# Kernel optimization log

Measured on AMD Instinct MI355X. Metric: run time of the kernel, lower is better.

The kernel has to match this reference:

```python
import jax, jax.numpy as jnp
import numpy as np

# Standard NF4 lookup table (16 quantile values of a normal distribution)
NF4_TABLE = jnp.array([
    -1.0, -0.6961928009986877, -0.5250730514526367, -0.39491748809814453,
    -0.28444138169288635, -0.18477343022823334, -0.09105003625154495, 0.0,
    0.07958029955625534, 0.16093020141124725, 0.24611230194568634,
    0.33791524171829224, 0.44070982933044434, 0.5626170039176941,
    0.7229568362236023, 1.0], dtype=jnp.float32)
BLOCK = 64  # per-block quantization block size


def dequant_nf4(codes, scalers):
    """codes: int [out, in] values in [0,16); scalers: float [out*in/BLOCK]."""
    shape = codes.shape
    vals = NF4_TABLE[codes.reshape(-1, BLOCK)]  # [n_blocks, BLOCK]
    return (vals * scalers[:, None]).reshape(shape)


def setup_inputs() -> dict:
    key = jax.random.key(0)
    ks = jax.random.split(key, 7)
    D, H, T = 4096, 11008, 8192
    nb1 = H * D // BLOCK
    x = jax.random.normal(ks[0], (T, D), dtype=jnp.float32)
    w1_codes = jax.random.randint(ks[1], (H, D), 0, 16, dtype=jnp.int32)
    w1_scalers = jax.random.uniform(ks[2], (nb1,), dtype=jnp.float32) * 0.02
    w2_codes = jax.random.randint(ks[3], (H, D), 0, 16, dtype=jnp.int32)
    w2_scalers = jax.random.uniform(ks[4], (nb1,), dtype=jnp.float32) * 0.02
    w3_codes = jax.random.randint(ks[5], (D, H), 0, 16, dtype=jnp.int32)
    w3_scalers = jax.random.uniform(ks[6], (nb1,), dtype=jnp.float32) * 0.02
    return {"x": x, "w1_codes": w1_codes, "w1_scalers": w1_scalers,
            "w2_codes": w2_codes, "w2_scalers": w2_scalers,
            "w3_codes": w3_codes, "w3_scalers": w3_scalers}


def reference(x, w1_codes, w1_scalers, w2_codes, w2_scalers, w3_codes, w3_scalers):
    w1 = dequant_nf4(w1_codes, w1_scalers)  # [H, D]
    w2 = dequant_nf4(w2_codes, w2_scalers)  # [H, D]
    w3 = dequant_nf4(w3_codes, w3_scalers)  # [D, H]
    h = jax.nn.silu(x @ w1.T) * (x @ w2.T)  # [T, H]
    return h @ w3.T                          # [T, D]
```

## Files before the change

### kernel.cpp

```cpp
#include <hip/hip_runtime.h>
#include <hip/hip_bf16.h>

#define T_DIM 8192
#define D_DIM 4096
#define H_DIM 11008

typedef __attribute__((ext_vector_type(8))) __bf16 bf16x8;
typedef __attribute__((ext_vector_type(4))) float f32x4;

typedef __attribute__((address_space(1))) const void gvoid_t;
typedef __attribute__((address_space(3))) void lvoid_t;

__device__ __forceinline__ void async_lds16(const void* g, void* l) {
    __builtin_amdgcn_global_load_lds((gvoid_t*)g, (lvoid_t*)l, 16, 0, 0);
}

__device__ const float NF4_TAB[16] = {
    -1.0f, -0.6961928009986877f, -0.5250730514526367f, -0.39491748809814453f,
    -0.28444138169288635f, -0.18477343022823334f, -0.09105003625154495f, 0.0f,
    0.07958029955625534f, 0.16093020141124725f, 0.24611230194568634f,
    0.33791524171829224f, 0.44070982933044434f, 0.5626170039176941f,
    0.7229568362236023f, 1.0f};

__global__ void dequant_nf4_kernel(const int* __restrict__ codes,
                                   const float* __restrict__ scalers,
                                   __bf16* __restrict__ out, long n) {
    __shared__ float tbl[16];
    if (threadIdx.x < 16) tbl[threadIdx.x] = NF4_TAB[threadIdx.x];
    __syncthreads();
    long i = ((long)blockIdx.x * blockDim.x + threadIdx.x) * 8;
    if (i >= n) return;
    float s = scalers[i >> 6];
    const int4* cp = (const int4*)(codes + i);
    int4 c0 = cp[0], c1 = cp[1];
    bf16x8 v;
    v[0] = (__bf16)(tbl[c0.x] * s);
    v[1] = (__bf16)(tbl[c0.y] * s);
    v[2] = (__bf16)(tbl[c0.z] * s);
    v[3] = (__bf16)(tbl[c0.w] * s);
    v[4] = (__bf16)(tbl[c1.x] * s);
    v[5] = (__bf16)(tbl[c1.y] * s);
    v[6] = (__bf16)(tbl[c1.z] * s);
    v[7] = (__bf16)(tbl[c1.w] * s);
    *(bf16x8*)(out + i) = v;
}

__global__ void cvt_f32_bf16(const float* __restrict__ x, __bf16* __restrict__ out, long n) {
    long i = ((long)blockIdx.x * blockDim.x + threadIdx.x) * 8;
    if (i >= n) return;
    const float4* xp = (const float4*)(x + i);
    float4 f0 = xp[0], f1 = xp[1];
    bf16x8 v;
    v[0] = (__bf16)f0.x; v[1] = (__bf16)f0.y; v[2] = (__bf16)f0.z; v[3] = (__bf16)f0.w;
    v[4] = (__bf16)f1.x; v[5] = (__bf16)f1.y; v[6] = (__bf16)f1.z; v[7] = (__bf16)f1.w;
    *(bf16x8*)(out + i) = v;
}

template<int KD, int FUSE, typename OutT>
__global__ __launch_bounds__(512, 2) void gemm_nt(
    const __bf16* __restrict__ A, const __bf16* __restrict__ B,
    const __bf16* __restrict__ A1, OutT* __restrict__ Out, const int N)
{
    static_assert(KD % 128 == 0, "need an even number of K-tiles");
    __shared__ __bf16 lds[2 * 2 * 256 * 64];

    const int tid  = threadIdx.x;
    const int lane = tid & 63;
    const int wave = tid >> 6;
    const int wm = wave >> 2;
    const int wn = wave & 3;

    const int nwg  = gridDim.x * gridDim.y;
    const int bid0 = blockIdx.y * gridDim.x + blockIdx.x;
    const int bid  = (bid0 & 7) * (nwg >> 3) + (bid0 >> 3);
    const int bx = bid % gridDim.x;
    const int by = bid / gridDim.x;
    const long m0 = (long)by * 256;
    const long n0 = (long)bx * 256;

    const int sr = tid >> 3;
    const int sb = (tid & 7) ^ (sr & 7);
    const __bf16* Arow = A + (m0 + sr) * (long)KD + sb * 8;
    const __bf16* Brow = B + (n0 + sr) * (long)KD + sb * 8;
    __bf16* dstA = &lds[(wave << 3) * 64];
    __bf16* dstB = dstA + 16384;

#define STAGE_A(BUF, H, KT) do { \
        const __bf16* s_ = Arow + (long)(H) * 128 * KD + (long)(KT) * 64; \
        __bf16* d_ = dstA + (BUF) * 32768 + (H) * 8192; \
        async_lds16(s_, d_); \
        async_lds16(s_ + 64 * (long)KD, d_ + 4096); \
    } while (0)
#define STAGE_B(BUF, H, KT) do { \
        const __bf16* s_ = Brow + (long)(H) * 128 * KD + (long)(KT) * 64; \
        __bf16* d_ = dstB + (BUF) * 32768 + (H) * 8192; \
        async_lds16(s_, d_); \
        async_lds16(s_ + 64 * (long)KD, d_ + 4096); \
    } while (0)

    const int r15 = lane & 15;
    const int hi2 = lane >> 4;
    const int l7  = lane & 7;
    const int aOff = (wm * 128 + r15) * 64;
    const int bOff = 16384 + (wn * 64 + r15) * 64;

    auto rdA = [&](int buf, int m, int kk) -> bf16x8 {
        return *(const bf16x8*)&lds[buf * 32768 + aOff + m * 1024 +
                                    (((kk * 4 + hi2) ^ l7) << 3)];
    };
    auto rdB = [&](int buf, int n, int kk) -> bf16x8 {
        return *(const bf16x8*)&lds[buf * 32768 + bOff + n * 1024 +
                                    (((kk * 4 + hi2) ^ l7) << 3)];
    };

    f32x4 acc[8][4];
    const f32x4 z4 = {0.f, 0.f, 0.f, 0.f};
#pragma unroll
    for (int m = 0; m < 8; ++m)
#pragma unroll
        for (int n = 0; n < 4; ++n) acc[m][n] = z4;

    bf16x8 aF[4][2];
    bf16x8 bF[4][2];

#define LOAD_A4(BUF, MB) { _Pragma("unroll") for (int m_ = 0; m_ < 4; ++m_) { \
        aF[m_][0] = rdA(BUF, m_ + MB, 0); aF[m_][1] = rdA(BUF, m_ + MB, 1); } }
#define LOAD_B2(BUF, NB) { _Pragma("unroll") for (int n_ = 0; n_ < 2; ++n_) { \
        bF[n_ + NB][0] = rdB(BUF, n_ + NB, 0); bF[n_ + NB][1] = rdB(BUF, n_ + NB, 1); } }
#define QUAD(MB, NB) { _Pragma("unroll") for (int m_ = 0; m_ < 4; ++m_) { \
        _Pragma("unroll") for (int n_ = 0; n_ < 2; ++n_) { \
        acc[m_ + MB][n_ + NB] = __builtin_amdgcn_mfma_f32_16x16x32_bf16( \
            aF[m_][0], bF[n_ + NB][0], acc[m_ + MB][n_ + NB], 0, 0, 0); \
        acc[m_ + MB][n_ + NB] = __builtin_amdgcn_mfma_f32_16x16x32_bf16( \
            aF[m_][1], bF[n_ + NB][1], acc[m_ + MB][n_ + NB], 0, 0, 0); } } }
#define BAR()  __builtin_amdgcn_s_barrier()
#define LGK0() asm volatile("s_waitcnt lgkmcnt(0)" ::: "memory")
#define VM4()  asm volatile("s_waitcnt vmcnt(4)" ::: "memory")
#define PRIO1() __builtin_amdgcn_s_setprio(1)
#define PRIO0() __builtin_amdgcn_s_setprio(0)

    const int NT = KD / 64;

    STAGE_A(0, 0, 0); STAGE_A(0, 1, 0);
    STAGE_B(0, 0, 0); STAGE_B(0, 1, 0);
    STAGE_B(1, 0, 1); STAGE_B(1, 1, 1);
    VM4();
    BAR();

#pragma unroll 1
    for (int t = 0; t < NT; t += 2) {
        const int t1 = t + 1;
        int t2 = t + 2; if (t2 >= NT) t2 -= NT;
        int t3 = t + 3; if (t3 >= NT) t3 -= NT;

        LOAD_A4(0, 0); LOAD_B2(0, 0);
        STAGE_A(1, 0, t1);
        BAR(); LGK0();
        PRIO1(); QUAD(0, 0); PRIO0();
        BAR();

        LOAD_B2(0, 2);
        STAGE_A(1, 1, t1);
        BAR(); LGK0();
        PRIO1(); QUAD(0, 2); PRIO0();
        BAR();

        LOAD_A4(0, 4);
        STAGE_B(0, 0, t2);
        BAR(); LGK0();
        PRIO1(); QUAD(4, 2); PRIO0();
        BAR();

        STAGE_B(0, 1, t2);
        BAR();
        PRIO1(); QUAD(4, 0); PRIO0();
        VM4();
        BAR();

        LOAD_A4(1, 0); LOAD_B2(1, 0);
        STAGE_A(0, 0, t2);
        BAR(); LGK0();
        PRIO1(); QUAD(0, 0); PRIO0();
        BAR();

        LOAD_B2(1, 2);
        STAGE_A(0, 1, t2);
        BAR(); LGK0();
        PRIO1(); QUAD(0, 2); PRIO0();
        BAR();

        LOAD_A4(1, 4);
        STAGE_B(1, 0, t3);
        BAR(); LGK0();
        PRIO1(); QUAD(4, 2); PRIO0();
        BAR();

        STAGE_B(1, 1, t3);
        BAR();
        PRIO1(); QUAD(4, 0); PRIO0();
        VM4();
        BAR();
    }
    asm volatile("s_waitcnt vmcnt(0)" ::: "memory");

    const int crow = hi2 * 4;
#pragma unroll
    for (int m = 0; m < 8; ++m)
#pragma unroll
        for (int n = 0; n < 4; ++n)
#pragma unroll
            for (int r = 0; r < 4; ++r) {
                const long row = m0 + wm * 128 + m * 16 + crow + r;
                const long idx = row * (long)N + (n0 + wn * 64 + n * 16 + r15);
                float a = acc[m][n][r];
                if (FUSE) {
                    float b = (float)A1[idx];
                    float sg = 1.0f / (1.0f + __expf(-a));
                    Out[idx] = (OutT)(a * sg * b);
                } else {
                    Out[idx] = (OutT)a;
                }
            }
#undef STAGE_A
#undef STAGE_B
#undef LOAD_A4
#undef LOAD_B2
#undef QUAD
#undef BAR
#undef LGK0
#undef VM4
#undef PRIO1
#undef PRIO0
}

extern "C" void kernel_launch(void* const* d_in, const int* in_sizes, int n_in,
                              void* d_out, int out_size, void* d_ws, size_t ws_size,
                              hipStream_t stream) {
    const float* x   = (const float*)d_in[0];
    const int*   w1c = (const int*)d_in[1];
    const float* w1s = (const float*)d_in[2];
    const int*   w2c = (const int*)d_in[3];
    const float* w2s = (const float*)d_in[4];
    const int*   w3c = (const int*)d_in[5];
    const float* w3s = (const float*)d_in[6];
    float* out = (float*)d_out;

    char* ws = (char*)d_ws;
    __bf16* xb  = (__bf16*)ws;  ws += (size_t)T_DIM * D_DIM * 2;
    __bf16* w1b = (__bf16*)ws;  ws += (size_t)H_DIM * D_DIM * 2;
    __bf16* w2b = (__bf16*)ws;  ws += (size_t)H_DIM * D_DIM * 2;
    __bf16* w3b = (__bf16*)ws;  ws += (size_t)H_DIM * D_DIM * 2;
    __bf16* hb  = (__bf16*)ws;

    const long nx = (long)T_DIM * D_DIM;
    const long nw = (long)H_DIM * D_DIM;

    cvt_f32_bf16<<<(int)(nx / (256 * 8)), 256, 0, stream>>>(x, xb, nx);
    dequant_nf4_kernel<<<(int)(nw / (256 * 8)), 256, 0, stream>>>(w1c, w1s, w1b, nw);
    dequant_nf4_kernel<<<(int)(nw / (256 * 8)), 256, 0, stream>>>(w2c, w2s, w2b, nw);
    dequant_nf4_kernel<<<(int)(nw / (256 * 8)), 256, 0, stream>>>(w3c, w3s, w3b, nw);

    gemm_nt<D_DIM, 0, __bf16><<<dim3(H_DIM / 256, T_DIM / 256), 512, 0, stream>>>(
        xb, w2b, nullptr, hb, H_DIM);
    gemm_nt<D_DIM, 1, __bf16><<<dim3(H_DIM / 256, T_DIM / 256), 512, 0, stream>>>(
        xb, w1b, hb, hb, H_DIM);
    gemm_nt<H_DIM, 0, float><<<dim3(D_DIM / 256, T_DIM / 256), 512, 0, stream>>>(
        hb, w3b, nullptr, out, D_DIM);
}
```

Measured before the change: 2.443 ms.

## Fuse gate and up projections into one GEMM with interleaved B tiles

Merges the two separate x@w2 and x@w1 GEMMs into a single kernel. Each 256-wide B tile now interleaves 16-row slices of w1 and w2, so SiLU(a)*b is computed straight from the accumulators. This removes the intermediate write and read of h between the two launches and stages each x tile into LDS only once for both projections. It also restructures the K-loop pipeline into a TILE macro with a different staging order and vmcnt(6) wait, which holds more A fragments in registers and may add register pressure.

```diff
diff --git a/kernel.cpp b/kernel.cpp
--- a/kernel.cpp
+++ b/kernel.cpp
@@ -56,10 +56,10 @@
     *(bf16x8*)(out + i) = v;
 }
 
-template<int KD, int FUSE, typename OutT>
+template<int KD, int SILU, typename OutT>
 __global__ __launch_bounds__(512, 2) void gemm_nt(
-    const __bf16* __restrict__ A, const __bf16* __restrict__ B,
-    const __bf16* __restrict__ A1, OutT* __restrict__ Out, const int N)
+    const __bf16* __restrict__ A, const __bf16* __restrict__ B1,
+    const __bf16* __restrict__ B2, OutT* __restrict__ Out, const int N)
 {
     static_assert(KD % 128 == 0, "need an even number of K-tiles");
     __shared__ __bf16 lds[2 * 2 * 256 * 64];
@@ -76,14 +76,23 @@
     const int bx = bid % gridDim.x;
     const int by = bid / gridDim.x;
     const long m0 = (long)by * 256;
-    const long n0 = (long)bx * 256;
+    const long n0 = (long)bx * (SILU ? 128 : 256);
 
     const int sr = tid >> 3;
     const int sb = (tid & 7) ^ (sr & 7);
     const __bf16* Arow = A + (m0 + sr) * (long)KD + sb * 8;
-    const __bf16* Brow = B + (n0 + sr) * (long)KD + sb * 8;
+    const __bf16* Brow;
+    if (SILU) {
+        const __bf16* matp = (sr & 16) ? B2 : B1;
+        Brow = matp + (n0 + ((sr >> 5) << 4) + (sr & 15)) * (long)KD + sb * 8;
+    } else {
+        Brow = B1 + (n0 + sr) * (long)KD + sb * 8;
+    }
     __bf16* dstA = &lds[(wave << 3) * 64];
     __bf16* dstB = dstA + 16384;
+
+    const long BH = (SILU ? 64 : 128) * (long)KD;
+    const long BA = (SILU ? 32 : 64) * (long)KD;
 
 #define STAGE_A(BUF, H, KT) do { \
         const __bf16* s_ = Arow + (long)(H) * 128 * KD + (long)(KT) * 64; \
@@ -92,10 +101,10 @@
         async_lds16(s_ + 64 * (long)KD, d_ + 4096); \
     } while (0)
 #define STAGE_B(BUF, H, KT) do { \
-        const __bf16* s_ = Brow + (long)(H) * 128 * KD + (long)(KT) * 64; \
+        const __bf16* s_ = Brow + (long)(H) * BH + (long)(KT) * 64; \
         __bf16* d_ = dstB + (BUF) * 32768 + (H) * 8192; \
         async_lds16(s_, d_); \
-        async_lds16(s_ + 64 * (long)KD, d_ + 4096); \
+        async_lds16(s_ + BA, d_ + 4096); \
     } while (0)
 
     const int r15 = lane & 15;
@@ -120,31 +129,46 @@
 #pragma unroll
         for (int n = 0; n < 4; ++n) acc[m][n] = z4;
 
-    bf16x8 aF[4][2];
+    bf16x8 aF[8][2];
     bf16x8 bF[4][2];
 
 #define LOAD_A4(BUF, MB) { _Pragma("unroll") for (int m_ = 0; m_ < 4; ++m_) { \
-        aF[m_][0] = rdA(BUF, m_ + MB, 0); aF[m_][1] = rdA(BUF, m_ + MB, 1); } }
+        aF[m_ + MB][0] = rdA(BUF, m_ + MB, 0); \
+        aF[m_ + MB][1] = rdA(BUF, m_ + MB, 1); } }
 #define LOAD_B2(BUF, NB) { _Pragma("unroll") for (int n_ = 0; n_ < 2; ++n_) { \
-        bF[n_ + NB][0] = rdB(BUF, n_ + NB, 0); bF[n_ + NB][1] = rdB(BUF, n_ + NB, 1); } }
+        bF[n_ + NB][0] = rdB(BUF, n_ + NB, 0); \
+        bF[n_ + NB][1] = rdB(BUF, n_ + NB, 1); } }
 #define QUAD(MB, NB) { _Pragma("unroll") for (int m_ = 0; m_ < 4; ++m_) { \
         _Pragma("unroll") for (int n_ = 0; n_ < 2; ++n_) { \
         acc[m_ + MB][n_ + NB] = __builtin_amdgcn_mfma_f32_16x16x32_bf16( \
-            aF[m_][0], bF[n_ + NB][0], acc[m_ + MB][n_ + NB], 0, 0, 0); \
+            aF[m_ + MB][0], bF[n_ + NB][0], acc[m_ + MB][n_ + NB], 0, 0, 0); \
         acc[m_ + MB][n_ + NB] = __builtin_amdgcn_mfma_f32_16x16x32_bf16( \
-            aF[m_][1], bF[n_ + NB][1], acc[m_ + MB][n_ + NB], 0, 0, 0); } } }
+            aF[m_ + MB][1], bF[n_ + NB][1], acc[m_ + MB][n_ + NB], 0, 0, 0); } } }
 #define BAR()  __builtin_amdgcn_s_barrier()
 #define LGK0() asm volatile("s_waitcnt lgkmcnt(0)" ::: "memory")
-#define VM4()  asm volatile("s_waitcnt vmcnt(4)" ::: "memory")
+#define VM6()  asm volatile("s_waitcnt vmcnt(6)" ::: "memory")
 #define PRIO1() __builtin_amdgcn_s_setprio(1)
 #define PRIO0() __builtin_amdgcn_s_setprio(0)
 
+#define TILE(BUF, T1, T2) \
+    LOAD_A4(BUF, 0); LOAD_B2(BUF, 0); \
+    STAGE_B(1 - (BUF), 1, T1); \
+    BAR(); LGK0(); PRIO1(); QUAD(0, 0); PRIO0(); BAR(); \
+    LOAD_A4(BUF, 4); LOAD_B2(BUF, 2); \
+    BAR(); LGK0(); PRIO1(); QUAD(0, 2); PRIO0(); BAR(); \
+    STAGE_A(BUF, 0, T2); STAGE_A(BUF, 1, T2); \
+    PRIO1(); QUAD(4, 2); PRIO0(); \
+    STAGE_B(BUF, 0, T2); \
+    PRIO1(); QUAD(4, 0); PRIO0(); \
+    VM6(); BAR();
+
     const int NT = KD / 64;
 
     STAGE_A(0, 0, 0); STAGE_A(0, 1, 0);
     STAGE_B(0, 0, 0); STAGE_B(0, 1, 0);
-    STAGE_B(1, 0, 1); STAGE_B(1, 1, 1);
-    VM4();
+    STAGE_A(1, 0, 1); STAGE_A(1, 1, 1);
+    STAGE_B(1, 0, 1);
+    VM6();
     BAR();
 
 #pragma unroll 1
@@ -152,83 +176,47 @@
         const int t1 = t + 1;
         int t2 = t + 2; if (t2 >= NT) t2 -= NT;
         int t3 = t + 3; if (t3 >= NT) t3 -= NT;
-
-        LOAD_A4(0, 0); LOAD_B2(0, 0);
-        STAGE_A(1, 0, t1);
-        BAR(); LGK0();
-        PRIO1(); QUAD(0, 0); PRIO0();
-        BAR();
-
-        LOAD_B2(0, 2);
-        STAGE_A(1, 1, t1);
-        BAR(); LGK0();
-        PRIO1(); QUAD(0, 2); PRIO0();
-        BAR();
-
-        LOAD_A4(0, 4);
-        STAGE_B(0, 0, t2);
-        BAR(); LGK0();
-        PRIO1(); QUAD(4, 2); PRIO0();
-        BAR();
-
-        STAGE_B(0, 1, t2);
-        BAR();
-        PRIO1(); QUAD(4, 0); PRIO0();
-        VM4();
-        BAR();
-
-        LOAD_A4(1, 0); LOAD_B2(1, 0);
-        STAGE_A(0, 0, t2);
-        BAR(); LGK0();
-        PRIO1(); QUAD(0, 0); PRIO0();
-        BAR();
-
-        LOAD_B2(1, 2);
-        STAGE_A(0, 1, t2);
-        BAR(); LGK0();
-        PRIO1(); QUAD(0, 2); PRIO0();
-        BAR();
-
-        LOAD_A4(1, 4);
-        STAGE_B(1, 0, t3);
-        BAR(); LGK0();
-        PRIO1(); QUAD(4, 2); PRIO0();
-        BAR();
-
-        STAGE_B(1, 1, t3);
-        BAR();
-        PRIO1(); QUAD(4, 0); PRIO0();
-        VM4();
-        BAR();
+        TILE(0, t1, t2);
+        TILE(1, t2, t3);
     }
     asm volatile("s_waitcnt vmcnt(0)" ::: "memory");
 
     const int crow = hi2 * 4;
-#pragma unroll
-    for (int m = 0; m < 8; ++m)
-#pragma unroll
-        for (int n = 0; n < 4; ++n)
-#pragma unroll
-            for (int r = 0; r < 4; ++r) {
-                const long row = m0 + wm * 128 + m * 16 + crow + r;
-                const long idx = row * (long)N + (n0 + wn * 64 + n * 16 + r15);
-                float a = acc[m][n][r];
-                if (FUSE) {
-                    float b = (float)A1[idx];
+    if (SILU) {
+#pragma unroll
+        for (int m = 0; m < 8; ++m)
+#pragma unroll
+            for (int p = 0; p < 2; ++p)
+#pragma unroll
+                for (int r = 0; r < 4; ++r) {
+                    const long row = m0 + wm * 128 + m * 16 + crow + r;
+                    const long idx = row * (long)N + (n0 + wn * 32 + p * 16 + r15);
+                    float a = acc[m][2 * p][r];
+                    float b = acc[m][2 * p + 1][r];
                     float sg = 1.0f / (1.0f + __expf(-a));
                     Out[idx] = (OutT)(a * sg * b);
-                } else {
-                    Out[idx] = (OutT)a;
                 }
-            }
+    } else {
+#pragma unroll
+        for (int m = 0; m < 8; ++m)
+#pragma unroll
+            for (int n = 0; n < 4; ++n)
+#pragma unroll
+                for (int r = 0; r < 4; ++r) {
+                    const long row = m0 + wm * 128 + m * 16 + crow + r;
+                    const long idx = row * (long)N + (n0 + wn * 64 + n * 16 + r15);
+                    Out[idx] = (OutT)acc[m][n][r];
+                }
+    }
 #undef STAGE_A
 #undef STAGE_B
 #undef LOAD_A4
 #undef LOAD_B2
 #undef QUAD
+#undef TILE
 #undef BAR
 #undef LGK0
-#undef VM4
+#undef VM6
 #undef PRIO1
 #undef PRIO0
 }
@@ -260,10 +248,8 @@
     dequant_nf4_kernel<<<(int)(nw / (256 * 8)), 256, 0, stream>>>(w2c, w2s, w2b, nw);
     dequant_nf4_kernel<<<(int)(nw / (256 * 8)), 256, 0, stream>>>(w3c, w3s, w3b, nw);
 
-    gemm_nt<D_DIM, 0, __bf16><<<dim3(H_DIM / 256, T_DIM / 256), 512, 0, stream>>>(
-        xb, w2b, nullptr, hb, H_DIM);
-    gemm_nt<D_DIM, 1, __bf16><<<dim3(H_DIM / 256, T_DIM / 256), 512, 0, stream>>>(
-        xb, w1b, hb, hb, H_DIM);
+    gemm_nt<D_DIM, 1, __bf16><<<dim3(H_DIM / 128, T_DIM / 256), 512, 0, stream>>>(
+        xb, w1b, w2b, hb, H_DIM);
     gemm_nt<H_DIM, 0, float><<<dim3(D_DIM / 256, T_DIM / 256), 512, 0, stream>>>(
         hb, w3b, nullptr, out, D_DIM);
 }
```

Result: faster. 2.350 ms (-3.8%).
